# Kernel tuning notes

Hardware: AMD Instinct MI355X
Metric: run time of the kernel (lower is better)

The kernel has to match this reference:

```python
import jax, jax.numpy as jnp
import numpy as np

B, S, H = 4, 2048, 2048          # batch, seq_len, hidden_size
NH, NKV, D = 8, 1, 256           # query heads, kv heads (MQA), head_dim
ROPE_THETA = 10000.0
SCALE = D ** -0.5


def setup_inputs() -> dict:
    key = jax.random.key(0)
    k1, k2, k3 = jax.random.split(key, 3)
    hidden_states = jax.random.normal(k1, (B, S, H), dtype=jnp.float32)
    w_qkv = jax.random.normal(k2, (H, (NH + 2 * NKV) * D), dtype=jnp.float32) * 0.02
    w_o = jax.random.normal(k3, (NH * D, H), dtype=jnp.float32) * 0.02
    positions = jnp.arange(S, dtype=jnp.int32)
    return {"hidden_states": hidden_states, "positions": positions,
            "w_qkv": w_qkv, "w_o": w_o}


def _apply_rope(x, positions):
    # x: [B, S, n_heads, D], neox style: rotate halves
    d2 = D // 2
    inv_freq = 1.0 / (ROPE_THETA ** (jnp.arange(0, d2, dtype=jnp.float32) * 2.0 / D))
    ang = positions.astype(jnp.float32)[:, None] * inv_freq[None, :]      # [S, d2]
    cos = jnp.cos(ang)[None, :, None, :]                                  # [1,S,1,d2]
    sin = jnp.sin(ang)[None, :, None, :]
    x1, x2 = x[..., :d2], x[..., d2:]
    return jnp.concatenate([x1 * cos - x2 * sin, x2 * cos + x1 * sin], axis=-1)


def reference(hidden_states, positions, w_qkv, w_o):
    # fused QKV projection
    qkv = jnp.einsum('bsh,hd->bsd', hidden_states, w_qkv)                 # [B,S,(NH+2NKV)*D]
    q_size, kv_size = NH * D, NKV * D
    q = qkv[..., :q_size].reshape(B, S, NH, D)
    k = qkv[..., q_size:q_size + kv_size].reshape(B, S, NKV, D)
    v = qkv[..., q_size + kv_size:].reshape(B, S, NKV, D)

    q = _apply_rope(q, positions)
    k = _apply_rope(k, positions)

    # expand KV heads for MQA/GQA
    rep = NH // NKV
    k = jnp.repeat(k, rep, axis=2)                                        # [B,S,NH,D]
    v = jnp.repeat(v, rep, axis=2)

    scores = jnp.einsum('bqhd,bkhd->bhqk', q, k) * SCALE                  # [B,NH,S,S]
    causal = jnp.tril(jnp.ones((S, S), dtype=bool))
    scores = jnp.where(causal[None, None], scores, jnp.finfo(scores.dtype).min)
    probs = jax.nn.softmax(scores, axis=-1)
    attn = jnp.einsum('bhqk,bkhd->bqhd', probs, v).reshape(B, S, NH * D)

    return jnp.einsum('bsd,dh->bsh', attn, w_o)                           # [B,S,H]
```

## Files before the change

### kernel.cpp

```cpp
#include <hip/hip_runtime.h>
#include <math.h>

constexpr int BATCH = 4;
constexpr int SEQ   = 2048;
constexpr int HID   = 2048;
constexpr int NHEAD = 8;
constexpr int HD    = 256;
constexpr int QKVN  = (NHEAD + 2) * HD;
constexpr float SCL = 0.0625f;

typedef __bf16 bf16_t;
typedef __bf16 bf16x8 __attribute__((ext_vector_type(8)));
typedef float  f32x4  __attribute__((ext_vector_type(4)));

__device__ __forceinline__ f32x4 zero4() {
  f32x4 z; z[0] = 0.f; z[1] = 0.f; z[2] = 0.f; z[3] = 0.f; return z;
}

__device__ __forceinline__ f32x4 mfma16(bf16x8 a, bf16x8 b, f32x4 c) {
  return __builtin_amdgcn_mfma_f32_16x16x32_bf16(a, b, c, 0, 0, 0);
}

__device__ __forceinline__ void gl2lds16(const void* g, void* lds) {
  typedef __attribute__((address_space(1))) void* gp_t;
  typedef __attribute__((address_space(3))) void* lp_t;
  __builtin_amdgcn_global_load_lds((gp_t)(size_t)g,
                                   (lp_t)(unsigned int)(size_t)lds, 16, 0, 0);
}

__device__ __forceinline__ float rmax16(float v) {
#pragma unroll
  for (int o = 1; o < 16; o <<= 1) v = fmaxf(v, __shfl_xor(v, o));
  return v;
}
__device__ __forceinline__ float rsum16(float v) {
#pragma unroll
  for (int o = 1; o < 16; o <<= 1) v += __shfl_xor(v, o);
  return v;
}

__global__ __launch_bounds__(256)
void cvt_bf16_kernel(const float* __restrict__ in, bf16_t* __restrict__ out) {
  const int i = blockIdx.x * 256 + threadIdx.x;
  const float4 a = ((const float4*)in)[i * 2];
  const float4 b = ((const float4*)in)[i * 2 + 1];
  bf16x8 o;
  o[0] = (bf16_t)a.x; o[1] = (bf16_t)a.y; o[2] = (bf16_t)a.z; o[3] = (bf16_t)a.w;
  o[4] = (bf16_t)b.x; o[5] = (bf16_t)b.y; o[6] = (bf16_t)b.z; o[7] = (bf16_t)b.w;
  ((bf16x8*)out)[i] = o;
}

__global__ __launch_bounds__(256)
void transw_kernel(const float* __restrict__ w, bf16_t* __restrict__ wT, int K, int N) {
  __shared__ __align__(16) bf16_t tile[64][72];
  const int n0 = blockIdx.x * 64, k0 = blockIdx.y * 64;
  const int t = threadIdx.x, rr = t >> 3, c8 = (t & 7) * 8;
#pragma unroll
  for (int it = 0; it < 2; ++it) {
    const int r = rr + it * 32;
    const float4* p = (const float4*)(w + (size_t)(k0 + r) * N + n0 + c8);
    const float4 a = p[0], b = p[1];
    bf16x8 o;
    o[0] = (bf16_t)a.x; o[1] = (bf16_t)a.y; o[2] = (bf16_t)a.z; o[3] = (bf16_t)a.w;
    o[4] = (bf16_t)b.x; o[5] = (bf16_t)b.y; o[6] = (bf16_t)b.z; o[7] = (bf16_t)b.w;
    *(bf16x8*)&tile[r][c8] = o;
  }
  __syncthreads();
#pragma unroll
  for (int it = 0; it < 2; ++it) {
    const int rn = rr + it * 32;
    bf16x8 o;
#pragma unroll
    for (int j = 0; j < 8; ++j) o[j] = tile[c8 + j][rn];
    *(bf16x8*)&wT[(size_t)(n0 + rn) * K + k0 + c8] = o;
  }
}

#define BAR()   __builtin_amdgcn_s_barrier()
#define LGKM0() do { asm volatile("s_waitcnt lgkmcnt(0)" ::: "memory"); \
                     __builtin_amdgcn_sched_barrier(0); } while (0)
#define VMC(n)  asm volatile("s_waitcnt vmcnt(" #n ")" ::: "memory")

template <typename TC>
__global__ __launch_bounds__(512)
void gemm256_kernel(const bf16_t* __restrict__ A, const bf16_t* __restrict__ BT,
                    TC* __restrict__ C, int M, int N, int K) {
  __shared__ __align__(16) bf16_t As[2][2][128 * 64];
  __shared__ __align__(16) bf16_t Bs[2][2][128 * 64];

  const int tid = threadIdx.x;
  const int w = tid >> 6, lane = tid & 63;
  const int wr = w >> 2, wc = w & 3;
  const int quad = lane >> 4, l15 = lane & 15;
  const int bm = blockIdx.y * 256, bn = blockIdx.x * 256;

  const int srow = tid >> 3;
  const int sc16 = (tid & 7) ^ (srow & 7);
  const bf16_t* Asrc = A  + (size_t)(bm + srow) * K + sc16 * 8;
  const bf16_t* Bsrc = BT + (size_t)(bn + srow) * K + sc16 * 8;

#define STAGE_A(t, h) do {                                                  \
    const bf16_t* _s = Asrc + (size_t)((h) * 128) * K + (t) * 64;           \
    gl2lds16(_s,                 &As[(t) & 1][h][w * 512]);                 \
    gl2lds16(_s + (size_t)64 * K, &As[(t) & 1][h][4096 + w * 512]);         \
  } while (0)
#define STAGE_B(t, h) do {                                                  \
    const bf16_t* _s = Bsrc + (size_t)((h) * 128) * K + (t) * 64;           \
    gl2lds16(_s,                 &Bs[(t) & 1][h][w * 512]);                 \
    gl2lds16(_s + (size_t)64 * K, &Bs[(t) & 1][h][4096 + w * 512]);         \
  } while (0)

  const int c0  = ((quad ^ (l15 & 7)) << 3);
  const int aro = l15 * 64;
  const int bh  = wc >> 1;
  const int bro = ((wc & 1) * 64 + l15) * 64;

  f32x4 acc[8][4];
#pragma unroll
  for (int mt = 0; mt < 8; ++mt)
#pragma unroll
    for (int nt = 0; nt < 4; ++nt) acc[mt][nt] = zero4();

  bf16x8 bfr[4][2], a01[2][2], a2[6][2];

#define LD_B(b) do { _Pragma("unroll")                                      \
    for (int nt = 0; nt < 4; ++nt) {                                        \
      bfr[nt][0] = *(const bf16x8*)&Bs[b][bh][bro + nt * 1024 + c0];        \
      bfr[nt][1] = *(const bf16x8*)&Bs[b][bh][bro + nt * 1024 + (c0 ^ 32)]; \
    } } while (0)
#define LD_A01(b) do { _Pragma("unroll")                                    \
    for (int mt = 0; mt < 2; ++mt) {                                        \
      a01[mt][0] = *(const bf16x8*)&As[b][wr][aro + mt * 1024 + c0];        \
      a01[mt][1] = *(const bf16x8*)&As[b][wr][aro + mt * 1024 + (c0 ^ 32)]; \
    } } while (0)
#define LD_A2(b) do { _Pragma("unroll")                                     \
    for (int i = 0; i < 6; ++i) {                                           \
      a2[i][0] = *(const bf16x8*)&As[b][wr][aro + (i + 2) * 1024 + c0];     \
      a2[i][1] = *(const bf16x8*)&As[b][wr][aro + (i + 2) * 1024 + (c0^32)];\
    } } while (0)
#define MFMA8(A0, A1, mb) do {                                              \
    __builtin_amdgcn_s_setprio(1);                                          \
    _Pragma("unroll")                                                       \
    for (int nt = 0; nt < 4; ++nt) {                                        \
      acc[(mb)][nt]     = mfma16((A0)[0], bfr[nt][0], acc[(mb)][nt]);       \
      acc[(mb)][nt]     = mfma16((A0)[1], bfr[nt][1], acc[(mb)][nt]);       \
      acc[(mb)+1][nt]   = mfma16((A1)[0], bfr[nt][0], acc[(mb)+1][nt]);     \
      acc[(mb)+1][nt]   = mfma16((A1)[1], bfr[nt][1], acc[(mb)+1][nt]);     \
    }                                                                       \
    __builtin_amdgcn_s_setprio(0);                                          \
  } while (0)

  const int NITER = K >> 7;

  STAGE_A(0, 0); STAGE_A(0, 1); STAGE_B(0, 0); STAGE_B(0, 1);
  STAGE_A(1, 0); STAGE_A(1, 1);
  VMC(4);
  BAR();

  for (int u = 0; u < NITER; ++u) {
    const bool last = (u == NITER - 1);
    const int t1 = 2 * u + 1, t2 = 2 * u + 2, t3 = 2 * u + 3;

    LD_B(0); LD_A01(0);
    STAGE_B(t1, 0);
    BAR(); LGKM0();
    MFMA8(a01[0], a01[1], 0);
    BAR();
    LD_A2(0);
    STAGE_B(t1, 1);
    BAR(); LGKM0();
    MFMA8(a2[0], a2[1], 2);
    BAR();
    if (!last) STAGE_A(t2, 0);
    BAR();
    MFMA8(a2[2], a2[3], 4);
    BAR();
    if (!last) { STAGE_A(t2, 1); VMC(4); } else { VMC(0); }
    BAR();
    MFMA8(a2[4], a2[5], 6);
    BAR();
    LD_B(1); LD_A01(1);
    if (!last) STAGE_B(t2, 0);
    BAR(); LGKM0();
    MFMA8(a01[0], a01[1], 0);
    BAR();
    LD_A2(1);
    if (!last) STAGE_B(t2, 1);
    BAR(); LGKM0();
    MFMA8(a2[0], a2[1], 2);
    BAR();
    if (!last) STAGE_A(t3, 0);
    BAR();
    MFMA8(a2[2], a2[3], 4);
    BAR();
    if (!last) { STAGE_A(t3, 1); VMC(4); }
    BAR();
    MFMA8(a2[4], a2[5], 6);
    BAR();
  }

#pragma unroll
  for (int mt = 0; mt < 8; ++mt)
#pragma unroll
    for (int nt = 0; nt < 4; ++nt)
#pragma unroll
      for (int r = 0; r < 4; ++r) {
        const int row = bm + wr * 128 + mt * 16 + quad * 4 + r;
        const int col = bn + wc * 64 + nt * 16 + l15;
        C[(size_t)row * N + col] = (TC)acc[mt][nt][r];
      }
#undef STAGE_A
#undef STAGE_B
#undef LD_B
#undef LD_A01
#undef LD_A2
#undef MFMA8
}

__global__ __launch_bounds__(128)
void rope_table_kernel(const int* __restrict__ pos, float2* __restrict__ tab) {
  const int s = blockIdx.x, i = threadIdx.x;
  const float inv_freq = powf(10000.0f, -(float)i / 128.0f);
  const float ang = (float)pos[s] * inv_freq;
  float sn, cs;
  sincosf(ang, &sn, &cs);
  tab[s * 128 + i] = make_float2(cs, sn);
}

__global__ __launch_bounds__(256)
void rope_kernel(const float2* __restrict__ tab, bf16_t* __restrict__ qkv) {
  const int bs = blockIdx.x * 16 + (threadIdx.x >> 4);
  const int h  = blockIdx.y;
  const int i0 = (threadIdx.x & 15) * 8;
  const int s  = bs & (SEQ - 1);
  const size_t base = (size_t)bs * QKVN + (size_t)h * HD;
  bf16x8 a = *(const bf16x8*)&qkv[base + i0];
  bf16x8 b = *(const bf16x8*)&qkv[base + 128 + i0];
  bf16x8 oa, ob;
#pragma unroll
  for (int j = 0; j < 8; ++j) {
    const float2 t = tab[s * 128 + i0 + j];
    const float x1 = (float)a[j], x2 = (float)b[j];
    oa[j] = (bf16_t)(x1 * t.x - x2 * t.y);
    ob[j] = (bf16_t)(x2 * t.x + x1 * t.y);
  }
  *(bf16x8*)&qkv[base + i0]       = oa;
  *(bf16x8*)&qkv[base + 128 + i0] = ob;
}

__global__ __launch_bounds__(256)
void vtrans_kernel(const bf16_t* __restrict__ qkv, bf16_t* __restrict__ Vt) {
  __shared__ __align__(16) bf16_t tile[64][72];
  const int s0 = blockIdx.x * 64, d0 = blockIdx.y * 64, b = blockIdx.z;
  const int t = threadIdx.x, rr = t >> 3, c8 = (t & 7) * 8;
#pragma unroll
  for (int it = 0; it < 2; ++it) {
    const int r = rr + it * 32;
    *(bf16x8*)&tile[r][c8] =
        *(const bf16x8*)&qkv[(size_t)(b * SEQ + s0 + r) * QKVN + 2304 + d0 + c8];
  }
  __syncthreads();
#pragma unroll
  for (int it = 0; it < 2; ++it) {
    const int dd = rr + it * 32;
    bf16x8 o;
#pragma unroll
    for (int j = 0; j < 8; ++j) o[j] = tile[c8 + j][dd];
    *(bf16x8*)&Vt[(size_t)(b * HD + d0 + dd) * SEQ + s0 + c8] = o;
  }
}

__global__ __launch_bounds__(512)
void attn_kernel(const bf16_t* __restrict__ qkv, const bf16_t* __restrict__ Vt,
                 bf16_t* __restrict__ O) {
  __shared__ __align__(16) bf16_t Ks[2][64 * 256];
  __shared__ __align__(16) bf16_t Vts[2][256 * 64];
  __shared__ __align__(16) bf16_t Pl[8][16][72];

  const int tid = threadIdx.x, w = tid >> 6, lane = tid & 63;
  const int quad = lane >> 4, l15 = lane & 15;
  const int b = blockIdx.x >> 6;
  const int qtR = blockIdx.x & 63;
  const int h = w;

  const int krow_base = w * 2 + (lane >> 5);
  const int kcol = lane & 31;
  const int vrow_base = w * 8 + (lane >> 3);
  const int vcol = lane & 7;

  const bf16_t* kbase0 = qkv + (size_t)(b * SEQ) * QKVN + 2048;
  const bf16_t* vbase0 = Vt + (size_t)b * HD * SEQ;

  auto stage = [&](int kt, int buf) {
    const bf16_t* kbase = kbase0 + (size_t)(kt * 64) * QKVN;
#pragma unroll
    for (int i = 0; i < 4; ++i) {
      const int r = i * 16 + krow_base;
      gl2lds16(kbase + (size_t)r * QKVN + ((kcol ^ (r & 31)) << 3),
               &Ks[buf][(i * 512 + w * 64) * 8]);
    }
    const bf16_t* vbase = vbase0 + kt * 64;
#pragma unroll
    for (int i = 0; i < 4; ++i) {
      const int r = i * 64 + vrow_base;
      gl2lds16(vbase + (size_t)r * SEQ + ((vcol ^ (r & 7)) << 3),
               &Vts[buf][(i * 512 + w * 64) * 8]);
    }
  };

  for (int phase = 0; phase < 2; ++phase) {
    const int qt = phase ? (127 - qtR) : qtR;
    const int q0 = qt * 16;

    bf16x8 qf[8];
    const bf16_t* qp =
        qkv + (size_t)(b * SEQ + q0 + l15) * QKVN + (size_t)h * HD + quad * 8;
#pragma unroll
    for (int ks = 0; ks < 8; ++ks) qf[ks] = *(const bf16x8*)(qp + ks * 32);

    float mrun[4], lrun[4];
    f32x4 of[16];
#pragma unroll
    for (int r = 0; r < 4; ++r) { mrun[r] = -3e38f; lrun[r] = 0.f; }
#pragma unroll
    for (int dt = 0; dt < 16; ++dt) of[dt] = zero4();

    const int ntiles = q0 / 64 + 1;
    int cur = 0;
    stage(0, 0);
    __syncthreads();

    for (int kt = 0; kt < ntiles; ++kt) {
      if (kt + 1 < ntiles) stage(kt + 1, cur ^ 1);

      const bf16_t* ksb = Ks[cur];
      const bf16_t* vsb = Vts[cur];

      f32x4 sf[4];
#pragma unroll
      for (int nt = 0; nt < 4; ++nt) {
        f32x4 acc = zero4();
        const int row = nt * 16 + l15;
#pragma unroll
        for (int ks = 0; ks < 8; ++ks) {
          const int j = ks * 4 + quad;
          const bf16x8 kf = *(const bf16x8*)&ksb[row * 256 + ((j ^ (row & 31)) << 3)];
          acc = mfma16(qf[ks], kf, acc);
        }
        sf[nt] = acc;
      }

      const bool lastTile = (kt == ntiles - 1);
      float mx[4];
#pragma unroll
      for (int r = 0; r < 4; ++r) {
        const int qg = q0 + quad * 4 + r;
        float v = -3e38f;
#pragma unroll
        for (int nt = 0; nt < 4; ++nt) {
          float s = sf[nt][r] * SCL;
          if (lastTile) {
            const int kg = kt * 64 + nt * 16 + l15;
            if (kg > qg) s = -3e38f;
          }
          sf[nt][r] = s;
          v = fmaxf(v, s);
        }
        mx[r] = rmax16(v);
      }

      float g = 0.f;
#pragma unroll
      for (int r = 0; r < 4; ++r) g = fmaxf(g, mx[r] - mrun[r]);
      const bool resc = !__all(g <= 8.0f);
      f32x4 av;
      if (resc) {
#pragma unroll
        for (int r = 0; r < 4; ++r) {
          const float mn = fmaxf(mrun[r], mx[r]);
          av[r] = __expf(mrun[r] - mn);
          mrun[r] = mn;
          lrun[r] *= av[r];
        }
      }

#pragma unroll
      for (int r = 0; r < 4; ++r) {
        float sum = 0.f;
#pragma unroll
        for (int nt = 0; nt < 4; ++nt) {
          const float pv = __expf(sf[nt][r] - mrun[r]);
          Pl[w][quad * 4 + r][nt * 16 + l15] = (bf16_t)pv;
          sum += pv;
        }
        lrun[r] += rsum16(sum);
      }
      if (resc) {
#pragma unroll
        for (int dt = 0; dt < 16; ++dt) of[dt] *= av;
      }
      __asm__ volatile("s_waitcnt lgkmcnt(0)" ::: "memory");

      bf16x8 pa[2];
#pragma unroll
      for (int k2 = 0; k2 < 2; ++k2)
        pa[k2] = *(const bf16x8*)&Pl[w][l15][k2 * 32 + quad * 8];
#pragma unroll
      for (int dt = 0; dt < 16; ++dt) {
        const int row = dt * 16 + l15;
#pragma unroll
        for (int k2 = 0; k2 < 2; ++k2) {
          const int j = k2 * 4 + quad;
          const bf16x8 vf = *(const bf16x8*)&vsb[row * 64 + ((j ^ (row & 7)) << 3)];
          of[dt] = mfma16(pa[k2], vf, of[dt]);
        }
      }

      __syncthreads();
      cur ^= 1;
    }

    f32x4 iv;
#pragma unroll
    for (int r = 0; r < 4; ++r) iv[r] = 1.0f / lrun[r];
#pragma unroll
    for (int dt = 0; dt < 16; ++dt) {
      const f32x4 o = of[dt] * iv;
#pragma unroll
      for (int r = 0; r < 4; ++r)
        O[(size_t)(b * SEQ + q0 + quad * 4 + r) * HID + (size_t)h * HD + dt * 16 + l15] =
            (bf16_t)o[r];
    }
  }
}

extern "C" void kernel_launch(void* const* d_in, const int* in_sizes, int n_in,
                              void* d_out, int out_size, void* d_ws, size_t ws_size,
                              hipStream_t stream) {
  const float* hidden  = (const float*)d_in[0];
  const int* positions = (const int*)d_in[1];
  const float* w_qkv   = (const float*)d_in[2];
  const float* w_o     = (const float*)d_in[3];
  float* out           = (float*)d_out;

  char* ws = (char*)d_ws;
  bf16_t* hiddenB = (bf16_t*)ws; ws += (size_t)8192 * 2048 * 2;
  bf16_t* wqkvT   = (bf16_t*)ws; ws += (size_t)2560 * 2048 * 2;
  bf16_t* woT     = (bf16_t*)ws; ws += (size_t)2048 * 2048 * 2;
  bf16_t* qkvB    = (bf16_t*)ws; ws += (size_t)8192 * 2560 * 2;
  bf16_t* VtB     = (bf16_t*)ws; ws += (size_t)4 * 256 * 2048 * 2;
  bf16_t* attnB   = (bf16_t*)ws;

  float2* ropeTab = (float2*)attnB;

  cvt_bf16_kernel<<<8192, 256, 0, stream>>>(hidden, hiddenB);
  transw_kernel<<<dim3(QKVN / 64, HID / 64), 256, 0, stream>>>(w_qkv, wqkvT, HID, QKVN);
  transw_kernel<<<dim3(HID / 64, HID / 64), 256, 0, stream>>>(w_o, woT, HID, HID);
  rope_table_kernel<<<SEQ, 128, 0, stream>>>(positions, ropeTab);

  gemm256_kernel<bf16_t><<<dim3(QKVN / 256, 8192 / 256), 512, 0, stream>>>
      (hiddenB, wqkvT, qkvB, 8192, QKVN, HID);

  rope_kernel<<<dim3(BATCH * SEQ / 16, 9), 256, 0, stream>>>(ropeTab, qkvB);
  vtrans_kernel<<<dim3(SEQ / 64, HD / 64, BATCH), 256, 0, stream>>>(qkvB, VtB);

  attn_kernel<<<256, 512, 0, stream>>>(qkvB, VtB, attnB);

  gemm256_kernel<float><<<dim3(HID / 256, 8192 / 256), 512, 0, stream>>>
      (attnB, woT, out, 8192, HID, HID);
}
```

Baseline: 474.2 us.

## Split attention phases into separate blocks, drop LDS double buffering, swizzle P tile

The attention kernel no longer processes two paired query tiles per block. It launches twice as many blocks, each handling one query tile, and removes the double-buffered K/V staging so shared memory per block is halved. This lets more blocks be resident per CU for latency hiding. The P scratch buffer drops its padding and uses an XOR swizzle to avoid bank conflicts. The trade-off is that global-to-LDS loads are no longer overlapped with compute inside a block, and causal load balancing now depends on the hardware scheduler rather than explicit pairing.

```diff
diff --git a/kernel.cpp b/kernel.cpp
--- a/kernel.cpp
+++ b/kernel.cpp
@@ -273,15 +273,18 @@
 __global__ __launch_bounds__(512)
 void attn_kernel(const bf16_t* __restrict__ qkv, const bf16_t* __restrict__ Vt,
                  bf16_t* __restrict__ O) {
-  __shared__ __align__(16) bf16_t Ks[2][64 * 256];
-  __shared__ __align__(16) bf16_t Vts[2][256 * 64];
-  __shared__ __align__(16) bf16_t Pl[8][16][72];
+  __shared__ __align__(16) bf16_t Ks[64 * 256];
+  __shared__ __align__(16) bf16_t Vts[256 * 64];
+  __shared__ __align__(16) bf16_t Pl[8][16][64];
 
   const int tid = threadIdx.x, w = tid >> 6, lane = tid & 63;
   const int quad = lane >> 4, l15 = lane & 15;
-  const int b = blockIdx.x >> 6;
-  const int qtR = blockIdx.x & 63;
+  const int bid = blockIdx.x;
+  const int j = bid & 255;
+  const int b = j >> 6;
+  const int qt = (bid >> 8) ? (127 - (j & 63)) : (j & 63);
   const int h = w;
+  const int q0 = qt * 16;
 
   const int krow_base = w * 2 + (lane >> 5);
   const int kcol = lane & 31;
@@ -291,146 +294,133 @@
   const bf16_t* kbase0 = qkv + (size_t)(b * SEQ) * QKVN + 2048;
   const bf16_t* vbase0 = Vt + (size_t)b * HD * SEQ;
 
-  auto stage = [&](int kt, int buf) {
+  bf16x8 qf[8];
+  const bf16_t* qp =
+      qkv + (size_t)(b * SEQ + q0 + l15) * QKVN + (size_t)h * HD + quad * 8;
+#pragma unroll
+  for (int ks = 0; ks < 8; ++ks) qf[ks] = *(const bf16x8*)(qp + ks * 32);
+
+  float mrun[4], lrun[4];
+  f32x4 of[16];
+#pragma unroll
+  for (int r = 0; r < 4; ++r) { mrun[r] = -3e38f; lrun[r] = 0.f; }
+#pragma unroll
+  for (int dt = 0; dt < 16; ++dt) of[dt] = zero4();
+
+  const int ntiles = q0 / 64 + 1;
+
+  for (int kt = 0; kt < ntiles; ++kt) {
     const bf16_t* kbase = kbase0 + (size_t)(kt * 64) * QKVN;
 #pragma unroll
     for (int i = 0; i < 4; ++i) {
       const int r = i * 16 + krow_base;
       gl2lds16(kbase + (size_t)r * QKVN + ((kcol ^ (r & 31)) << 3),
-               &Ks[buf][(i * 512 + w * 64) * 8]);
+               &Ks[(i * 512 + w * 64) * 8]);
     }
     const bf16_t* vbase = vbase0 + kt * 64;
 #pragma unroll
     for (int i = 0; i < 4; ++i) {
       const int r = i * 64 + vrow_base;
       gl2lds16(vbase + (size_t)r * SEQ + ((vcol ^ (r & 7)) << 3),
-               &Vts[buf][(i * 512 + w * 64) * 8]);
-    }
-  };
-
-  for (int phase = 0; phase < 2; ++phase) {
-    const int qt = phase ? (127 - qtR) : qtR;
-    const int q0 = qt * 16;
-
-    bf16x8 qf[8];
-    const bf16_t* qp =
-        qkv + (size_t)(b * SEQ + q0 + l15) * QKVN + (size_t)h * HD + quad * 8;
-#pragma unroll
-    for (int ks = 0; ks < 8; ++ks) qf[ks] = *(const bf16x8*)(qp + ks * 32);
-
-    float mrun[4], lrun[4];
-    f32x4 of[16];
-#pragma unroll
-    for (int r = 0; r < 4; ++r) { mrun[r] = -3e38f; lrun[r] = 0.f; }
-#pragma unroll
-    for (int dt = 0; dt < 16; ++dt) of[dt] = zero4();
-
-    const int ntiles = q0 / 64 + 1;
-    int cur = 0;
-    stage(0, 0);
+               &Vts[(i * 512 + w * 64) * 8]);
+    }
     __syncthreads();
 
-    for (int kt = 0; kt < ntiles; ++kt) {
-      if (kt + 1 < ntiles) stage(kt + 1, cur ^ 1);
-
-      const bf16_t* ksb = Ks[cur];
-      const bf16_t* vsb = Vts[cur];
-
-      f32x4 sf[4];
+    f32x4 sf[4];
+#pragma unroll
+    for (int nt = 0; nt < 4; ++nt) {
+      f32x4 acc = zero4();
+      const int row = nt * 16 + l15;
+#pragma unroll
+      for (int ks = 0; ks < 8; ++ks) {
+        const int jj = ks * 4 + quad;
+        const bf16x8 kf = *(const bf16x8*)&Ks[row * 256 + ((jj ^ (row & 31)) << 3)];
+        acc = mfma16(qf[ks], kf, acc);
+      }
+      sf[nt] = acc;
+    }
+
+    const bool lastTile = (kt == ntiles - 1);
+    float mx[4];
+#pragma unroll
+    for (int r = 0; r < 4; ++r) {
+      const int qg = q0 + quad * 4 + r;
+      float v = -3e38f;
 #pragma unroll
       for (int nt = 0; nt < 4; ++nt) {
-        f32x4 acc = zero4();
-        const int row = nt * 16 + l15;
-#pragma unroll
-        for (int ks = 0; ks < 8; ++ks) {
-          const int j = ks * 4 + quad;
-          const bf16x8 kf = *(const bf16x8*)&ksb[row * 256 + ((j ^ (row & 31)) << 3)];
-          acc = mfma16(qf[ks], kf, acc);
+        float s = sf[nt][r] * SCL;
+        if (lastTile) {
+          const int kg = kt * 64 + nt * 16 + l15;
+          if (kg > qg) s = -3e38f;
         }
-        sf[nt] = acc;
-      }
-
-      const bool lastTile = (kt == ntiles - 1);
-      float mx[4];
+        sf[nt][r] = s;
+        v = fmaxf(v, s);
+      }
+      mx[r] = rmax16(v);
+    }
+
+    float g = 0.f;
+#pragma unroll
+    for (int r = 0; r < 4; ++r) g = fmaxf(g, mx[r] - mrun[r]);
+    const bool resc = !__all(g <= 8.0f);
+    f32x4 av;
+    if (resc) {
 #pragma unroll
       for (int r = 0; r < 4; ++r) {
-        const int qg = q0 + quad * 4 + r;
-        float v = -3e38f;
-#pragma unroll
-        for (int nt = 0; nt < 4; ++nt) {
-          float s = sf[nt][r] * SCL;
-          if (lastTile) {
-            const int kg = kt * 64 + nt * 16 + l15;
-            if (kg > qg) s = -3e38f;
-          }
-          sf[nt][r] = s;
-          v = fmaxf(v, s);
-        }
-        mx[r] = rmax16(v);
-      }
-
-      float g = 0.f;
-#pragma unroll
-      for (int r = 0; r < 4; ++r) g = fmaxf(g, mx[r] - mrun[r]);
-      const bool resc = !__all(g <= 8.0f);
-      f32x4 av;
-      if (resc) {
-#pragma unroll
-        for (int r = 0; r < 4; ++r) {
-          const float mn = fmaxf(mrun[r], mx[r]);
-          av[r] = __expf(mrun[r] - mn);
-          mrun[r] = mn;
-          lrun[r] *= av[r];
-        }
-      }
-
-#pragma unroll
-      for (int r = 0; r < 4; ++r) {
-        float sum = 0.f;
-#pragma unroll
-        for (int nt = 0; nt < 4; ++nt) {
-          const float pv = __expf(sf[nt][r] - mrun[r]);
-          Pl[w][quad * 4 + r][nt * 16 + l15] = (bf16_t)pv;
-          sum += pv;
-        }
-        lrun[r] += rsum16(sum);
-      }
-      if (resc) {
-#pragma unroll
-        for (int dt = 0; dt < 16; ++dt) of[dt] *= av;
-      }
-      __asm__ volatile("s_waitcnt lgkmcnt(0)" ::: "memory");
-
-      bf16x8 pa[2];
-#pragma unroll
-      for (int k2 = 0; k2 < 2; ++k2)
-        pa[k2] = *(const bf16x8*)&Pl[w][l15][k2 * 32 + quad * 8];
-#pragma unroll
-      for (int dt = 0; dt < 16; ++dt) {
-        const int row = dt * 16 + l15;
-#pragma unroll
-        for (int k2 = 0; k2 < 2; ++k2) {
-          const int j = k2 * 4 + quad;
-          const bf16x8 vf = *(const bf16x8*)&vsb[row * 64 + ((j ^ (row & 7)) << 3)];
-          of[dt] = mfma16(pa[k2], vf, of[dt]);
-        }
-      }
-
-      __syncthreads();
-      cur ^= 1;
-    }
-
-    f32x4 iv;
-#pragma unroll
-    for (int r = 0; r < 4; ++r) iv[r] = 1.0f / lrun[r];
+        const float mn = fmaxf(mrun[r], mx[r]);
+        av[r] = __expf(mrun[r] - mn);
+        mrun[r] = mn;
+        lrun[r] *= av[r];
+      }
+    }
+
+#pragma unroll
+    for (int r = 0; r < 4; ++r) {
+      const int rowp = quad * 4 + r;
+      float sum = 0.f;
+#pragma unroll
+      for (int nt = 0; nt < 4; ++nt) {
+        const float pv = __expf(sf[nt][r] - mrun[r]);
+        Pl[w][rowp][(((nt * 2 + (l15 >> 3)) ^ (rowp & 7)) << 3) + (l15 & 7)] =
+            (bf16_t)pv;
+        sum += pv;
+      }
+      lrun[r] += rsum16(sum);
+    }
+    if (resc) {
+#pragma unroll
+      for (int dt = 0; dt < 16; ++dt) of[dt] *= av;
+    }
+    __asm__ volatile("s_waitcnt lgkmcnt(0)" ::: "memory");
+
+    bf16x8 pa[2];
+#pragma unroll
+    for (int k2 = 0; k2 < 2; ++k2)
+      pa[k2] = *(const bf16x8*)&Pl[w][l15][(((k2 * 4 + quad) ^ (l15 & 7)) << 3)];
 #pragma unroll
     for (int dt = 0; dt < 16; ++dt) {
-      const f32x4 o = of[dt] * iv;
-#pragma unroll
-      for (int r = 0; r < 4; ++r)
-        O[(size_t)(b * SEQ + q0 + quad * 4 + r) * HID + (size_t)h * HD + dt * 16 + l15] =
-            (bf16_t)o[r];
-    }
+      const int row = dt * 16 + l15;
+#pragma unroll
+      for (int k2 = 0; k2 < 2; ++k2) {
+        const int jj = k2 * 4 + quad;
+        const bf16x8 vf = *(const bf16x8*)&Vts[row * 64 + ((jj ^ (row & 7)) << 3)];
+        of[dt] = mfma16(pa[k2], vf, of[dt]);
+      }
+    }
+
+    __syncthreads();
+  }
+
+  f32x4 iv;
+#pragma unroll
+  for (int r = 0; r < 4; ++r) iv[r] = 1.0f / lrun[r];
+#pragma unroll
+  for (int dt = 0; dt < 16; ++dt) {
+    const f32x4 o = of[dt] * iv;
+#pragma unroll
+    for (int r = 0; r < 4; ++r)
+      O[(size_t)(b * SEQ + q0 + quad * 4 + r) * HID + (size_t)h * HD + dt * 16 + l15] =
+          (bf16_t)o[r];
   }
 }
 
@@ -464,7 +454,7 @@
   rope_kernel<<<dim3(BATCH * SEQ / 16, 9), 256, 0, stream>>>(ropeTab, qkvB);
   vtrans_kernel<<<dim3(SEQ / 64, HD / 64, BATCH), 256, 0, stream>>>(qkvB, VtB);
 
-  attn_kernel<<<256, 512, 0, stream>>>(qkvB, VtB, attnB);
+  attn_kernel<<<512, 512, 0, stream>>>(qkvB, VtB, attnB);
 
   gemm256_kernel<float><<<dim3(HID / 256, 8192 / 256), 512, 0, stream>>>
       (attnB, woT, out, 8192, HID, HID);
```

Result: slower. 507.3 us (+7.0%).
